# Optimization experiments

Hardware: AMD Instinct MI355X
Metric: run time of the kernel (lower is better)

## Reference

```python
import jax, jax.numpy as jnp
import numpy as np

D = 512

def _layernorm(x, g, b, eps=1e-5):
    m = jnp.mean(x, axis=-1, keepdims=True)
    v = jnp.mean((x - m) ** 2, axis=-1, keepdims=True)
    return (x - m) / jnp.sqrt(v + eps) * g + b

def _bn_eval(x, g, b, eps=1e-5):
    # BatchNorm1d in eval mode with fresh buffers: running_mean=0, running_var=1
    return x / jnp.sqrt(1.0 + eps) * g + b

def setup_inputs() -> dict:
    key = jax.random.key(0)
    ks = jax.random.split(key, 8)
    B, V = 4096, 20
    s = 0.02
    return {
        "x":   jax.random.normal(ks[0], (B * V, D), jnp.float32),
        "We":  jax.random.normal(ks[1], (D, D), jnp.float32) * s,
        "be":  jnp.zeros((D,), jnp.float32),
        "W1":  jax.random.normal(ks[2], (D, D), jnp.float32) * s,
        "b1":  jnp.zeros((D,), jnp.float32),
        "Wa":  jax.random.normal(ks[3], (D, 1), jnp.float32) * s,
        "ba":  jnp.zeros((1,), jnp.float32),
        "W2":  jax.random.normal(ks[4], (D, D), jnp.float32) * s,
        "b2":  jnp.zeros((D,), jnp.float32),
        "ln_g": jnp.ones((D,), jnp.float32),
        "ln_b": jnp.zeros((D,), jnp.float32),
        "h1W": jax.random.normal(ks[5], (D, D), jnp.float32) * s,
        "h1b": jnp.zeros((D,), jnp.float32),
        "bn1_g": jnp.ones((D,), jnp.float32),
        "bn1_b": jnp.zeros((D,), jnp.float32),
        "h2W": jax.random.normal(ks[6], (D, 256), jnp.float32) * s,
        "h2b": jnp.zeros((256,), jnp.float32),
        "bn2_g": jnp.ones((256,), jnp.float32),
        "bn2_b": jnp.zeros((256,), jnp.float32),
        "h3W": jax.random.normal(ks[7], (256, 40), jnp.float32) * s,
        "h3b": jnp.zeros((40,), jnp.float32),
        "num_views": 20,
        "group_num": 8,
    }

def reference(x, We, be, W1, b1, Wa, ba, W2, b2, ln_g, ln_b,
              h1W, h1b, bn1_g, bn1_b, h2W, h2b, bn2_g, bn2_b, h3W, h3b,
              num_views, group_num):
    V = num_views
    f_cnn = x @ We + be                                  # [B*V, 512] stand-in encoder
    B = f_cnn.shape[0] // V
    xv = f_cnn.reshape(B, V, D)
    x1 = xv @ W1 + b1                                    # mlp1, [B, V, 512]
    f_vit1 = _layernorm(x1, ln_g, ln_b)
    att = jax.nn.sigmoid(f_vit1 @ Wa + ba)               # [B, V, 1], scores in (0,1)
    # group_pooling: bucket views by floor(score*group_num), max-pool per bucket,
    # then the forward takes max over the (non-empty) bucket maxes -- which is
    # exactly the max over all views of x1 (every view lands in one bucket).
    # bucket = clip(floor(att*group_num), 0, group_num-1)  # target for fused kernel
    f_vit2 = jnp.max(x1, axis=1)                         # [B, 512]
    f_vit2 = _layernorm(f_vit2 @ W2 + b2, ln_g, ln_b)    # mlp2 + shared norm
    h = _bn_eval(f_vit2 @ h1W + h1b, bn1_g, bn1_b)       # cls_head_finetune[:2]
    f_global = h
    h = jax.nn.relu(h)                                   # dropout = identity (eval)
    h = jax.nn.relu(_bn_eval(h @ h2W + h2b, bn2_g, bn2_b))
    pred = h @ h3W + h3b                                 # [B, 40]
    return (f_cnn.reshape(-1, D), f_vit1.reshape(-1, D), att.reshape(-1, V),
            f_vit2, f_global, pred)
```

## Files before the change

kernel.cpp:

```cpp
#include <hip/hip_runtime.h>
#include <cstdint>

typedef unsigned short u16;
typedef __bf16 bf16x8 __attribute__((ext_vector_type(8)));
typedef float f32x4 __attribute__((ext_vector_type(4)));

#define GLOBAL_AS __attribute__((address_space(1)))
#define LDS_AS __attribute__((address_space(3)))

__device__ __forceinline__ u16 f2bf(float f) {
  unsigned u = __builtin_bit_cast(unsigned, f);
  u += 0x7FFFu + ((u >> 16) & 1u);
  return (u16)(u >> 16);
}
__device__ __forceinline__ float bf2f(u16 h) {
  unsigned u = ((unsigned)h) << 16;
  return __builtin_bit_cast(float, u);
}
__device__ __forceinline__ void unpack2(unsigned u, float& a, float& b) {
  a = __builtin_bit_cast(float, u << 16);
  b = __builtin_bit_cast(float, u & 0xFFFF0000u);
}
__device__ __forceinline__ unsigned pk2(float a, float b) {
  return (unsigned)f2bf(a) | ((unsigned)f2bf(b) << 16);
}
__device__ __forceinline__ void gl_lds16(const void* g, void* l) {
  __builtin_amdgcn_global_load_lds((const GLOBAL_AS void*)g, (LDS_AS void*)l, 16, 0, 0);
}

__global__ __launch_bounds__(256) void transpose_w(const float* __restrict__ W,
                                                   u16* __restrict__ Wt, int K, int N) {
  __shared__ float tile[32][33];
  const int n0 = blockIdx.x * 32, k0 = blockIdx.y * 32;
  const int tx = threadIdx.x & 31, ty = threadIdx.x >> 5;
#pragma unroll
  for (int i = 0; i < 32; i += 8)
    tile[ty + i][tx] = W[(size_t)(k0 + ty + i) * N + n0 + tx];
  __syncthreads();
#pragma unroll
  for (int i = 0; i < 32; i += 8)
    Wt[(size_t)(n0 + ty + i) * K + k0 + tx] = f2bf(tile[tx][ty + i]);
}

template <int MODE, bool AF32>
__global__ __launch_bounds__(256) void gemm_k(
    const float* __restrict__ Af, const u16* __restrict__ Ab,
    const u16* __restrict__ Bt, const float* __restrict__ bias,
    float* __restrict__ outF, u16* __restrict__ outB,
    const float* __restrict__ bng, const float* __restrict__ bnb, int N) {
  __shared__ __align__(16) u16 As[128 * 32];
  __shared__ __align__(16) u16 Bs[128 * 32];
  const int t = threadIdx.x;
  const int tn0 = blockIdx.x * 128, tm0 = blockIdx.y * 128;
  const int w = t >> 6, lane = t & 63;
  const int wm = w >> 1, wn = w & 1, lr = lane & 15, quad = lane >> 4;

  f32x4 acc[4][4];
#pragma unroll
  for (int i = 0; i < 4; ++i)
#pragma unroll
    for (int j = 0; j < 4; ++j) {
      acc[i][j][0] = 0.f; acc[i][j][1] = 0.f; acc[i][j][2] = 0.f; acc[i][j][3] = 0.f;
    }

  for (int kc = 0; kc < 16; ++kc) {
    const int kb = kc * 32;
    {
      const int c0 = t, c1 = t + 256;
      gl_lds16(Bt + (size_t)(tn0 + (c0 >> 2)) * 512 + kb + (c0 & 3) * 8, Bs + c0 * 8);
      gl_lds16(Bt + (size_t)(tn0 + (c1 >> 2)) * 512 + kb + (c1 & 3) * 8, Bs + c1 * 8);
    }
    if constexpr (AF32) {
      const int row = t >> 1, half = t & 1;
      const float* g = Af + (size_t)(tm0 + row) * 512 + kb + half * 16;
      float4 q0 = ((const float4*)g)[0];
      float4 q1 = ((const float4*)g)[1];
      float4 q2 = ((const float4*)g)[2];
      float4 q3 = ((const float4*)g)[3];
      int4 s0 = make_int4(pk2(q0.x, q0.y), pk2(q0.z, q0.w), pk2(q1.x, q1.y), pk2(q1.z, q1.w));
      int4 s1 = make_int4(pk2(q2.x, q2.y), pk2(q2.z, q2.w), pk2(q3.x, q3.y), pk2(q3.z, q3.w));
      *(int4*)&As[row * 32 + half * 16] = s0;
      *(int4*)&As[row * 32 + half * 16 + 8] = s1;
    } else {
      const int c0 = t, c1 = t + 256;
      gl_lds16(Ab + (size_t)(tm0 + (c0 >> 2)) * 512 + kb + (c0 & 3) * 8, As + c0 * 8);
      gl_lds16(Ab + (size_t)(tm0 + (c1 >> 2)) * 512 + kb + (c1 & 3) * 8, As + c1 * 8);
    }
    __syncthreads();
    bf16x8 af[4], bfr[4];
#pragma unroll
    for (int mt = 0; mt < 4; ++mt)
      af[mt] = *(const bf16x8*)&As[(wm * 64 + mt * 16 + lr) * 32 + quad * 8];
#pragma unroll
    for (int nt = 0; nt < 4; ++nt)
      bfr[nt] = *(const bf16x8*)&Bs[(wn * 64 + nt * 16 + lr) * 32 + quad * 8];
#pragma unroll
    for (int mt = 0; mt < 4; ++mt)
#pragma unroll
      for (int nt = 0; nt < 4; ++nt)
        acc[mt][nt] = __builtin_amdgcn_mfma_f32_16x16x32_bf16(af[mt], bfr[nt], acc[mt][nt], 0, 0, 0);
    __syncthreads();
  }

  const float BNS = 0.9999950000374998f;
#pragma unroll
  for (int nt = 0; nt < 4; ++nt) {
    const int col = tn0 + wn * 64 + nt * 16 + lr;
    const float bs = bias[col];
    float g_ = 0.f, b_ = 0.f;
    if constexpr (MODE == 2 || MODE == 3) { g_ = bng[col] * BNS; b_ = bnb[col]; }
#pragma unroll
    for (int mt = 0; mt < 4; ++mt) {
      const int row0 = tm0 + wm * 64 + mt * 16 + quad * 4;
#pragma unroll
      for (int r = 0; r < 4; ++r) {
        const size_t idx = (size_t)(row0 + r) * N + col;
        const float v = acc[mt][nt][r] + bs;
        if constexpr (MODE == 0) {
          outB[idx] = f2bf(v);
        } else if constexpr (MODE == 1) {
          outF[idx] = v;
        } else if constexpr (MODE == 2) {
          const float y = v * g_ + b_;
          outF[idx] = y;
          outB[idx] = f2bf(fmaxf(y, 0.f));
        } else if constexpr (MODE == 3) {
          const float y = v * g_ + b_;
          outB[idx] = f2bf(fmaxf(y, 0.f));
        } else {
          outF[idx] = v;
          outB[idx] = f2bf(v);
        }
      }
    }
  }
}

__global__ __launch_bounds__(256) void fuse_ln_att_max(
    const u16* __restrict__ x1, const float* __restrict__ g, const float* __restrict__ bb,
    const float* __restrict__ Wa, const float* __restrict__ ba,
    float* __restrict__ fv1, float* __restrict__ att, u16* __restrict__ fv2raw) {
  __shared__ __align__(16) u16 xs[20 * 512];
  const int b = blockIdx.x, t = threadIdx.x;
  const int4* src = (const int4*)(x1 + (size_t)b * 10240);
  int4* dst = (int4*)xs;
#pragma unroll
  for (int i = 0; i < 5; ++i) dst[t + 256 * i] = src[t + 256 * i];
  __syncthreads();
  const int w = t >> 6, lane = t & 63;
  const float inv512 = 1.0f / 512.0f;
  const float ba0 = ba[0];
  float gv[8], bv[8], wv[8];
#pragma unroll
  for (int e = 0; e < 8; ++e) {
    gv[e] = g[lane * 8 + e];
    bv[e] = bb[lane * 8 + e];
    wv[e] = Wa[lane * 8 + e];
  }
#pragma unroll
  for (int j = 0; j < 5; ++j) {
    const int v = w * 5 + j;
    int4 q = *(const int4*)&xs[v * 512 + lane * 8];
    float f[8];
    unpack2((unsigned)q.x, f[0], f[1]);
    unpack2((unsigned)q.y, f[2], f[3]);
    unpack2((unsigned)q.z, f[4], f[5]);
    unpack2((unsigned)q.w, f[6], f[7]);
    float s = 0.f, ss = 0.f;
#pragma unroll
    for (int e = 0; e < 8; ++e) { s += f[e]; ss += f[e] * f[e]; }
#pragma unroll
    for (int o = 32; o; o >>= 1) { s += __shfl_xor(s, o); ss += __shfl_xor(ss, o); }
    const float m = s * inv512;
    const float var = ss * inv512 - m * m;
    const float rs = rsqrtf(var + 1e-5f);
    float y[8], z = 0.f;
#pragma unroll
    for (int e = 0; e < 8; ++e) {
      y[e] = (f[e] - m) * rs * gv[e] + bv[e];
      z += y[e] * wv[e];
    }
    float* op = fv1 + ((size_t)b * 20 + v) * 512 + lane * 8;
    *(float4*)op = make_float4(y[0], y[1], y[2], y[3]);
    *(float4*)(op + 4) = make_float4(y[4], y[5], y[6], y[7]);
#pragma unroll
    for (int o = 32; o; o >>= 1) z += __shfl_xor(z, o);
    if (lane == 0) att[(size_t)b * 20 + v] = 1.f / (1.f + __expf(-(z + ba0)));
  }
  for (int d = t; d < 512; d += 256) {
    float mx = -3.4e38f;
#pragma unroll
    for (int v = 0; v < 20; ++v) mx = fmaxf(mx, bf2f(xs[v * 512 + d]));
    fv2raw[(size_t)b * 512 + d] = f2bf(mx);
  }
}

__global__ __launch_bounds__(256) void ln_rows(const float* __restrict__ in,
                                               const float* __restrict__ g,
                                               const float* __restrict__ bb,
                                               float* __restrict__ outF, u16* __restrict__ outB) {
  const int row = blockIdx.x * 4 + (threadIdx.x >> 6);
  const int lane = threadIdx.x & 63;
  const float* p = in + (size_t)row * 512 + lane * 8;
  float4 a = *(const float4*)p, c = *(const float4*)(p + 4);
  float f[8] = {a.x, a.y, a.z, a.w, c.x, c.y, c.z, c.w};
  float s = 0.f, ss = 0.f;
#pragma unroll
  for (int e = 0; e < 8; ++e) { s += f[e]; ss += f[e] * f[e]; }
#pragma unroll
  for (int o = 32; o; o >>= 1) { s += __shfl_xor(s, o); ss += __shfl_xor(ss, o); }
  const float m = s * (1.0f / 512.0f);
  const float rs = rsqrtf(ss * (1.0f / 512.0f) - m * m + 1e-5f);
  float y[8];
#pragma unroll
  for (int e = 0; e < 8; ++e) y[e] = (f[e] - m) * rs * g[lane * 8 + e] + bb[lane * 8 + e];
  float* op = outF + (size_t)row * 512 + lane * 8;
  *(float4*)op = make_float4(y[0], y[1], y[2], y[3]);
  *(float4*)(op + 4) = make_float4(y[4], y[5], y[6], y[7]);
  int4 ob = make_int4(pk2(y[0], y[1]), pk2(y[2], y[3]), pk2(y[4], y[5]), pk2(y[6], y[7]));
  *(int4*)(outB + (size_t)row * 512 + lane * 8) = ob;
}

__global__ __launch_bounds__(320) void pred_k(const u16* __restrict__ h2a,
                                              const float* __restrict__ W,
                                              const float* __restrict__ bias,
                                              float* __restrict__ out) {
  const int t = threadIdx.x;
  const int r = t / 40, n = t - r * 40;
  const size_t b = (size_t)blockIdx.x * 8 + r;
  const u16* hp = h2a + b * 256;
  float s = 0.f;
#pragma unroll 4
  for (int k0 = 0; k0 < 256; k0 += 8) {
    int4 q = *(const int4*)(hp + k0);
    float f0, f1, f2, f3, f4, f5, f6, f7;
    unpack2((unsigned)q.x, f0, f1);
    unpack2((unsigned)q.y, f2, f3);
    unpack2((unsigned)q.z, f4, f5);
    unpack2((unsigned)q.w, f6, f7);
    const float* wp = W + (size_t)k0 * 40 + n;
    s += f0 * wp[0] + f1 * wp[40] + f2 * wp[80] + f3 * wp[120] +
         f4 * wp[160] + f5 * wp[200] + f6 * wp[240] + f7 * wp[280];
  }
  out[b * 40 + n] = s + bias[n];
}

extern "C" void kernel_launch(void* const* d_in, const int* in_sizes, int n_in,
                              void* d_out, int out_size, void* d_ws, size_t ws_size,
                              hipStream_t stream) {
  (void)in_sizes; (void)n_in; (void)out_size; (void)ws_size;
  const float* x    = (const float*)d_in[0];
  const float* We   = (const float*)d_in[1];
  const float* be   = (const float*)d_in[2];
  const float* W1   = (const float*)d_in[3];
  const float* b1   = (const float*)d_in[4];
  const float* Wa   = (const float*)d_in[5];
  const float* ba   = (const float*)d_in[6];
  const float* W2   = (const float*)d_in[7];
  const float* b2   = (const float*)d_in[8];
  const float* ln_g = (const float*)d_in[9];
  const float* ln_b = (const float*)d_in[10];
  const float* h1W  = (const float*)d_in[11];
  const float* h1b  = (const float*)d_in[12];
  const float* bn1g = (const float*)d_in[13];
  const float* bn1b = (const float*)d_in[14];
  const float* h2W  = (const float*)d_in[15];
  const float* h2b  = (const float*)d_in[16];
  const float* bn2g = (const float*)d_in[17];
  const float* bn2b = (const float*)d_in[18];
  const float* h3W  = (const float*)d_in[19];
  const float* h3b  = (const float*)d_in[20];

  float* out = (float*)d_out;
  float* o_fcnn  = out;
  float* o_fvit1 = o_fcnn + 41943040;
  float* o_att   = o_fvit1 + 41943040;
  float* o_fvit2 = o_att + 81920;
  float* o_fglob = o_fvit2 + 2097152;
  float* o_pred  = o_fglob + 2097152;

  u16* ws = (u16*)d_ws;
  u16* Wet   = ws;
  u16* W1t   = Wet + 262144;
  u16* W2t   = W1t + 262144;
  u16* h1Wt  = W2t + 262144;
  u16* h2Wt  = h1Wt + 262144;
  u16* fcnnB = h2Wt + 131072;
  u16* x1B   = fcnnB + 41943040;
  u16* fv2rB = x1B + 41943040;
  u16* fv2B  = fv2rB + 2097152;
  u16* hrelB = fv2B + 2097152;
  u16* h2aB  = hrelB + 2097152;
  float* t3raw = (float*)(h2aB + 1048576);

  const dim3 blk(256);
  transpose_w<<<dim3(16, 16), blk, 0, stream>>>(We, Wet, 512, 512);
  transpose_w<<<dim3(16, 16), blk, 0, stream>>>(W1, W1t, 512, 512);
  transpose_w<<<dim3(16, 16), blk, 0, stream>>>(W2, W2t, 512, 512);
  transpose_w<<<dim3(16, 16), blk, 0, stream>>>(h1W, h1Wt, 512, 512);
  transpose_w<<<dim3(8, 16), blk, 0, stream>>>(h2W, h2Wt, 512, 256);

  gemm_k<4, true><<<dim3(4, 640), blk, 0, stream>>>(x, nullptr, Wet, be, o_fcnn, fcnnB,
                                                    nullptr, nullptr, 512);
  gemm_k<0, false><<<dim3(4, 640), blk, 0, stream>>>(nullptr, fcnnB, W1t, b1, nullptr, x1B,
                                                     nullptr, nullptr, 512);
  fuse_ln_att_max<<<dim3(4096), blk, 0, stream>>>(x1B, ln_g, ln_b, Wa, ba, o_fvit1, o_att, fv2rB);
  gemm_k<1, false><<<dim3(4, 32), blk, 0, stream>>>(nullptr, fv2rB, W2t, b2, t3raw, nullptr,
                                                    nullptr, nullptr, 512);
  ln_rows<<<dim3(1024), blk, 0, stream>>>(t3raw, ln_g, ln_b, o_fvit2, fv2B);
  gemm_k<2, false><<<dim3(4, 32), blk, 0, stream>>>(nullptr, fv2B, h1Wt, h1b, o_fglob, hrelB,
                                                    bn1g, bn1b, 512);
  gemm_k<3, false><<<dim3(2, 32), blk, 0, stream>>>(nullptr, hrelB, h2Wt, h2b, nullptr, h2aB,
                                                    bn2g, bn2b, 256);
  pred_k<<<dim3(512), dim3(320), 0, stream>>>(h2aB, h3W, h3b, o_pred);
}
```

Before: 787.5 us.

## Fold encoder and mlp1 weights into one combined GEMM sharing the x tile

Precomputes Wc = We·W1 and a combined bias, so x1 is computed directly from x instead of from a bf16 copy of f_cnn. A new dual-output GEMM loads each x tile once and multiplies it against both We and Wc, which removes the bf16 f_cnn write and its re-read by a second large GEMM. The GEMMs also gain double-buffered LDS with register prefetch, an XOR swizzle on the A tile, block-index remapping, and smaller 64x64 tiles for the small tail GEMMs. In exchange x1 is rounded differently (the product of bf16 weights is itself rounded to bf16), and the fused kernel carries two accumulator sets, which raises register pressure.

Result: faster. 764.5 us (-2.9%).

```diff
diff --git a/kernel.cpp b/kernel.cpp
--- a/kernel.cpp
+++ b/kernel.cpp
@@ -42,95 +42,225 @@
     Wt[(size_t)(n0 + ty + i) * K + k0 + tx] = f2bf(tile[tx][ty + i]);
 }
 
-template <int MODE, bool AF32>
-__global__ __launch_bounds__(256) void gemm_k(
+__global__ __launch_bounds__(128) void bias_c(const float* __restrict__ be,
+                                              const float* __restrict__ W1,
+                                              const float* __restrict__ b1,
+                                              float* __restrict__ bc) {
+  const int n = blockIdx.x * 128 + threadIdx.x;
+  float s = b1[n];
+  for (int k = 0; k < 512; ++k) s += be[k] * W1[(size_t)k * 512 + n];
+  bc[n] = s;
+}
+
+template <int MODE, int FM, int FN, bool AF32>
+__global__ __launch_bounds__(256) void gemm_k2(
     const float* __restrict__ Af, const u16* __restrict__ Ab,
     const u16* __restrict__ Bt, const float* __restrict__ bias,
     float* __restrict__ outF, u16* __restrict__ outB,
     const float* __restrict__ bng, const float* __restrict__ bnb, int N) {
-  __shared__ __align__(16) u16 As[128 * 32];
-  __shared__ __align__(16) u16 Bs[128 * 32];
+  constexpr int TM = 32 * FM, TN = 32 * FN;
+  __shared__ __align__(16) u16 As[2][TM * 32];
+  __shared__ __align__(16) u16 Bs[2][TN * 32];
   const int t = threadIdx.x;
-  const int tn0 = blockIdx.x * 128, tm0 = blockIdx.y * 128;
+  const int tn0 = blockIdx.x * TN, tm0 = blockIdx.y * TM;
   const int w = t >> 6, lane = t & 63;
   const int wm = w >> 1, wn = w & 1, lr = lane & 15, quad = lane >> 4;
 
-  f32x4 acc[4][4];
-#pragma unroll
-  for (int i = 0; i < 4; ++i)
-#pragma unroll
-    for (int j = 0; j < 4; ++j) {
+  f32x4 acc[FM][FN];
+#pragma unroll
+  for (int i = 0; i < FM; ++i)
+#pragma unroll
+    for (int j = 0; j < FN; ++j) {
       acc[i][j][0] = 0.f; acc[i][j][1] = 0.f; acc[i][j][2] = 0.f; acc[i][j][3] = 0.f;
     }
 
+  float4 aq[4];
+  auto stage = [&](int buf, int kb) {
+#pragma unroll
+    for (int i = 0; i < TN / 64; ++i) {
+      const int c = t + 256 * i;
+      gl_lds16(Bt + (size_t)(tn0 + (c >> 2)) * 512 + kb + (c & 3) * 8, &Bs[buf][c * 8]);
+    }
+    if constexpr (!AF32) {
+#pragma unroll
+      for (int i = 0; i < TM / 64; ++i) {
+        const int c = t + 256 * i;
+        gl_lds16(Ab + (size_t)(tm0 + (c >> 2)) * 512 + kb + (c & 3) * 8, &As[buf][c * 8]);
+      }
+    }
+  };
+  auto loadA = [&](int kb) {
+    const int row = t >> 1, half = t & 1;
+    const float* g = Af + (size_t)(tm0 + row) * 512 + kb + half * 16;
+    aq[0] = ((const float4*)g)[0]; aq[1] = ((const float4*)g)[1];
+    aq[2] = ((const float4*)g)[2]; aq[3] = ((const float4*)g)[3];
+  };
+  auto writeA = [&](int buf) {
+    const int row = t >> 1, half = t & 1;
+    int4 s0 = make_int4(pk2(aq[0].x, aq[0].y), pk2(aq[0].z, aq[0].w),
+                        pk2(aq[1].x, aq[1].y), pk2(aq[1].z, aq[1].w));
+    int4 s1 = make_int4(pk2(aq[2].x, aq[2].y), pk2(aq[2].z, aq[2].w),
+                        pk2(aq[3].x, aq[3].y), pk2(aq[3].z, aq[3].w));
+    const int m = (row & 7) << 3;
+    *(int4*)&As[buf][(row * 32 + half * 16) ^ m] = s0;
+    *(int4*)&As[buf][(row * 32 + half * 16 + 8) ^ m] = s1;
+  };
+
+  if constexpr (AF32) { loadA(0); writeA(0); }
+  stage(0, 0);
+  __syncthreads();
+
   for (int kc = 0; kc < 16; ++kc) {
-    const int kb = kc * 32;
-    {
-      const int c0 = t, c1 = t + 256;
-      gl_lds16(Bt + (size_t)(tn0 + (c0 >> 2)) * 512 + kb + (c0 & 3) * 8, Bs + c0 * 8);
-      gl_lds16(Bt + (size_t)(tn0 + (c1 >> 2)) * 512 + kb + (c1 & 3) * 8, Bs + c1 * 8);
-    }
-    if constexpr (AF32) {
-      const int row = t >> 1, half = t & 1;
-      const float* g = Af + (size_t)(tm0 + row) * 512 + kb + half * 16;
-      float4 q0 = ((const float4*)g)[0];
-      float4 q1 = ((const float4*)g)[1];
-      float4 q2 = ((const float4*)g)[2];
-      float4 q3 = ((const float4*)g)[3];
-      int4 s0 = make_int4(pk2(q0.x, q0.y), pk2(q0.z, q0.w), pk2(q1.x, q1.y), pk2(q1.z, q1.w));
-      int4 s1 = make_int4(pk2(q2.x, q2.y), pk2(q2.z, q2.w), pk2(q3.x, q3.y), pk2(q3.z, q3.w));
-      *(int4*)&As[row * 32 + half * 16] = s0;
-      *(int4*)&As[row * 32 + half * 16 + 8] = s1;
-    } else {
-      const int c0 = t, c1 = t + 256;
-      gl_lds16(Ab + (size_t)(tm0 + (c0 >> 2)) * 512 + kb + (c0 & 3) * 8, As + c0 * 8);
-      gl_lds16(Ab + (size_t)(tm0 + (c1 >> 2)) * 512 + kb + (c1 & 3) * 8, As + c1 * 8);
+    const int cur = kc & 1;
+    if (kc < 15) {
+      if constexpr (AF32) loadA(kc * 32 + 32);
+      stage(cur ^ 1, kc * 32 + 32);
+    }
+    bf16x8 af[FM], bfr[FN];
+#pragma unroll
+    for (int mt = 0; mt < FM; ++mt) {
+      const int ar = wm * (TM / 2) + mt * 16 + lr;
+      const int idx = AF32 ? ((ar * 32 + quad * 8) ^ ((ar & 7) << 3)) : (ar * 32 + quad * 8);
+      af[mt] = *(const bf16x8*)&As[cur][idx];
+    }
+#pragma unroll
+    for (int nt = 0; nt < FN; ++nt)
+      bfr[nt] = *(const bf16x8*)&Bs[cur][(wn * (TN / 2) + nt * 16 + lr) * 32 + quad * 8];
+#pragma unroll
+    for (int mt = 0; mt < FM; ++mt)
+#pragma unroll
+      for (int nt = 0; nt < FN; ++nt)
+        acc[mt][nt] = __builtin_amdgcn_mfma_f32_16x16x32_bf16(af[mt], bfr[nt], acc[mt][nt], 0, 0, 0);
+    if (kc < 15) {
+      if constexpr (AF32) writeA(cur ^ 1);
     }
     __syncthreads();
-    bf16x8 af[4], bfr[4];
-#pragma unroll
-    for (int mt = 0; mt < 4; ++mt)
-      af[mt] = *(const bf16x8*)&As[(wm * 64 + mt * 16 + lr) * 32 + quad * 8];
-#pragma unroll
-    for (int nt = 0; nt < 4; ++nt)
-      bfr[nt] = *(const bf16x8*)&Bs[(wn * 64 + nt * 16 + lr) * 32 + quad * 8];
-#pragma unroll
-    for (int mt = 0; mt < 4; ++mt)
-#pragma unroll
-      for (int nt = 0; nt < 4; ++nt)
-        acc[mt][nt] = __builtin_amdgcn_mfma_f32_16x16x32_bf16(af[mt], bfr[nt], acc[mt][nt], 0, 0, 0);
-    __syncthreads();
   }
 
   const float BNS = 0.9999950000374998f;
 #pragma unroll
-  for (int nt = 0; nt < 4; ++nt) {
-    const int col = tn0 + wn * 64 + nt * 16 + lr;
-    const float bs = bias[col];
-    float g_ = 0.f, b_ = 0.f;
+  for (int nt = 0; nt < FN; ++nt) {
+    const int col = tn0 + wn * (TN / 2) + nt * 16 + lr;
+    float bs = 0.f, g_ = 0.f, b_ = 0.f;
+    if constexpr (MODE != 7) bs = bias[col];
     if constexpr (MODE == 2 || MODE == 3) { g_ = bng[col] * BNS; b_ = bnb[col]; }
 #pragma unroll
-    for (int mt = 0; mt < 4; ++mt) {
-      const int row0 = tm0 + wm * 64 + mt * 16 + quad * 4;
+    for (int mt = 0; mt < FM; ++mt) {
+      const int row0 = tm0 + wm * (TM / 2) + mt * 16 + quad * 4;
 #pragma unroll
       for (int r = 0; r < 4; ++r) {
-        const size_t idx = (size_t)(row0 + r) * N + col;
         const float v = acc[mt][nt][r] + bs;
-        if constexpr (MODE == 0) {
-          outB[idx] = f2bf(v);
-        } else if constexpr (MODE == 1) {
-          outF[idx] = v;
+        if constexpr (MODE == 1) {
+          outF[(size_t)(row0 + r) * N + col] = v;
         } else if constexpr (MODE == 2) {
           const float y = v * g_ + b_;
+          const size_t idx = (size_t)(row0 + r) * N + col;
           outF[idx] = y;
           outB[idx] = f2bf(fmaxf(y, 0.f));
         } else if constexpr (MODE == 3) {
           const float y = v * g_ + b_;
-          outB[idx] = f2bf(fmaxf(y, 0.f));
+          outB[(size_t)(row0 + r) * N + col] = f2bf(fmaxf(y, 0.f));
         } else {
-          outF[idx] = v;
-          outB[idx] = f2bf(v);
+          outB[(size_t)col * N + (row0 + r)] = f2bf(v);
         }
+      }
+    }
+  }
+}
+
+__global__ __launch_bounds__(256) void gemm_x2(
+    const float* __restrict__ x, const u16* __restrict__ B1t, const u16* __restrict__ B2t,
+    const float* __restrict__ b1v, const float* __restrict__ b2v,
+    float* __restrict__ outF, u16* __restrict__ outB) {
+  __shared__ __align__(16) u16 As[2][128 * 32];
+  __shared__ __align__(16) u16 B1s[2][128 * 32];
+  __shared__ __align__(16) u16 B2s[2][128 * 32];
+  const int t = threadIdx.x;
+  int bid = blockIdx.y * 4 + blockIdx.x;
+  bid = (bid & 7) * 320 + (bid >> 3);
+  const int tn0 = (bid & 3) * 128, tm0 = (bid >> 2) * 128;
+  const int w = t >> 6, lane = t & 63;
+  const int wm = w >> 1, wn = w & 1, lr = lane & 15, quad = lane >> 4;
+
+  f32x4 acc0[4][4], acc1[4][4];
+#pragma unroll
+  for (int i = 0; i < 4; ++i)
+#pragma unroll
+    for (int j = 0; j < 4; ++j) {
+      acc0[i][j][0] = 0.f; acc0[i][j][1] = 0.f; acc0[i][j][2] = 0.f; acc0[i][j][3] = 0.f;
+      acc1[i][j][0] = 0.f; acc1[i][j][1] = 0.f; acc1[i][j][2] = 0.f; acc1[i][j][3] = 0.f;
+    }
+
+  float4 aq[4];
+  auto stageB = [&](int buf, int kb) {
+#pragma unroll
+    for (int i = 0; i < 2; ++i) {
+      const int c = t + 256 * i;
+      const size_t go = (size_t)(tn0 + (c >> 2)) * 512 + kb + (c & 3) * 8;
+      gl_lds16(B1t + go, &B1s[buf][c * 8]);
+      gl_lds16(B2t + go, &B2s[buf][c * 8]);
+    }
+  };
+  auto loadA = [&](int kb) {
+    const int row = t >> 1, half = t & 1;
+    const float* g = x + (size_t)(tm0 + row) * 512 + kb + half * 16;
+    aq[0] = ((const float4*)g)[0]; aq[1] = ((const float4*)g)[1];
+    aq[2] = ((const float4*)g)[2]; aq[3] = ((const float4*)g)[3];
+  };
+  auto writeA = [&](int buf) {
+    const int row = t >> 1, half = t & 1;
+    int4 s0 = make_int4(pk2(aq[0].x, aq[0].y), pk2(aq[0].z, aq[0].w),
+                        pk2(aq[1].x, aq[1].y), pk2(aq[1].z, aq[1].w));
+    int4 s1 = make_int4(pk2(aq[2].x, aq[2].y), pk2(aq[2].z, aq[2].w),
+                        pk2(aq[3].x, aq[3].y), pk2(aq[3].z, aq[3].w));
+    const int m = (row & 7) << 3;
+    *(int4*)&As[buf][(row * 32 + half * 16) ^ m] = s0;
+    *(int4*)&As[buf][(row * 32 + half * 16 + 8) ^ m] = s1;
+  };
+
+  loadA(0); writeA(0); stageB(0, 0);
+  __syncthreads();
+
+  for (int kc = 0; kc < 16; ++kc) {
+    const int cur = kc & 1;
+    if (kc < 15) {
+      loadA(kc * 32 + 32);
+      stageB(cur ^ 1, kc * 32 + 32);
+    }
+    bf16x8 af[4];
+#pragma unroll
+    for (int mt = 0; mt < 4; ++mt) {
+      const int ar = wm * 64 + mt * 16 + lr;
+      af[mt] = *(const bf16x8*)&As[cur][(ar * 32 + quad * 8) ^ ((ar & 7) << 3)];
+    }
+#pragma unroll
+    for (int nt = 0; nt < 4; ++nt) {
+      const int bi = (wn * 64 + nt * 16 + lr) * 32 + quad * 8;
+      bf16x8 b1 = *(const bf16x8*)&B1s[cur][bi];
+#pragma unroll
+      for (int mt = 0; mt < 4; ++mt)
+        acc0[mt][nt] = __builtin_amdgcn_mfma_f32_16x16x32_bf16(af[mt], b1, acc0[mt][nt], 0, 0, 0);
+      bf16x8 b2 = *(const bf16x8*)&B2s[cur][bi];
+#pragma unroll
+      for (int mt = 0; mt < 4; ++mt)
+        acc1[mt][nt] = __builtin_amdgcn_mfma_f32_16x16x32_bf16(af[mt], b2, acc1[mt][nt], 0, 0, 0);
+    }
+    if (kc < 15) writeA(cur ^ 1);
+    __syncthreads();
+  }
+
+#pragma unroll
+  for (int nt = 0; nt < 4; ++nt) {
+    const int col = tn0 + wn * 64 + nt * 16 + lr;
+    const float bsE = b1v[col], bsC = b2v[col];
+#pragma unroll
+    for (int mt = 0; mt < 4; ++mt) {
+      const int row0 = tm0 + wm * 64 + mt * 16 + quad * 4;
+#pragma unroll
+      for (int r = 0; r < 4; ++r) {
+        const size_t idx = (size_t)(row0 + r) * 512 + col;
+        outF[idx] = acc0[mt][nt][r] + bsE;
+        outB[idx] = f2bf(acc1[mt][nt][r] + bsC);
       }
     }
   }
@@ -285,13 +415,14 @@
   u16* W2t   = W1t + 262144;
   u16* h1Wt  = W2t + 262144;
   u16* h2Wt  = h1Wt + 262144;
-  u16* fcnnB = h2Wt + 131072;
-  u16* x1B   = fcnnB + 41943040;
+  u16* Wct   = h2Wt + 131072;
+  u16* x1B   = Wct + 262144;
   u16* fv2rB = x1B + 41943040;
   u16* fv2B  = fv2rB + 2097152;
   u16* hrelB = fv2B + 2097152;
   u16* h2aB  = hrelB + 2097152;
-  float* t3raw = (float*)(h2aB + 1048576);
+  float* bc    = (float*)(h2aB + 1048576);
+  float* t3raw = bc + 512;
 
   const dim3 blk(256);
   transpose_w<<<dim3(16, 16), blk, 0, stream>>>(We, Wet, 512, 512);
@@ -300,17 +431,20 @@
   transpose_w<<<dim3(16, 16), blk, 0, stream>>>(h1W, h1Wt, 512, 512);
   transpose_w<<<dim3(8, 16), blk, 0, stream>>>(h2W, h2Wt, 512, 256);
 
-  gemm_k<4, true><<<dim3(4, 640), blk, 0, stream>>>(x, nullptr, Wet, be, o_fcnn, fcnnB,
-                                                    nullptr, nullptr, 512);
-  gemm_k<0, false><<<dim3(4, 640), blk, 0, stream>>>(nullptr, fcnnB, W1t, b1, nullptr, x1B,
-                                                     nullptr, nullptr, 512);
+  gemm_k2<7, 4, 4, true><<<dim3(4, 4), blk, 0, stream>>>(
+      We, nullptr, W1t, nullptr, nullptr, Wct, nullptr, nullptr, 512);
+  bias_c<<<dim3(4), dim3(128), 0, stream>>>(be, W1, b1, bc);
+
+  gemm_x2<<<dim3(4, 640), blk, 0, stream>>>(x, Wet, Wct, be, bc, o_fcnn, x1B);
+
   fuse_ln_att_max<<<dim3(4096), blk, 0, stream>>>(x1B, ln_g, ln_b, Wa, ba, o_fvit1, o_att, fv2rB);
-  gemm_k<1, false><<<dim3(4, 32), blk, 0, stream>>>(nullptr, fv2rB, W2t, b2, t3raw, nullptr,
-                                                    nullptr, nullptr, 512);
+
+  gemm_k2<1, 2, 2, false><<<dim3(8, 64), blk, 0, stream>>>(
+      nullptr, fv2rB, W2t, b2, t3raw, nullptr, nullptr, nullptr, 512);
   ln_rows<<<dim3(1024), blk, 0, stream>>>(t3raw, ln_g, ln_b, o_fvit2, fv2B);
-  gemm_k<2, false><<<dim3(4, 32), blk, 0, stream>>>(nullptr, fv2B, h1Wt, h1b, o_fglob, hrelB,
-                                                    bn1g, bn1b, 512);
-  gemm_k<3, false><<<dim3(2, 32), blk, 0, stream>>>(nullptr, hrelB, h2Wt, h2b, nullptr, h2aB,
-                                                    bn2g, bn2b, 256);
+  gemm_k2<2, 2, 2, false><<<dim3(8, 64), blk, 0, stream>>>(
+      nullptr, fv2B, h1Wt, h1b, o_fglob, hrelB, bn1g, bn1b, 512);
+  gemm_k2<3, 2, 2, false><<<dim3(4, 64), blk, 0, stream>>>(
+      nullptr, hrelB, h2Wt, h2b, nullptr, h2aB, bn2g, bn2b, 256);
   pred_k<<<dim3(512), dim3(320), 0, stream>>>(h2aB, h3W, h3b, o_pred);
 }
```
